# Kernel tuning notes

Measured on AMD Instinct MI355X. Metric: run time of the kernel, lower is better.

Reference implementation:

```python
import jax, jax.numpy as jnp
import numpy as np

N = 50000
E = 800000
D = 128
H = 8
DH = D // H


def setup_inputs() -> dict:
    key = jax.random.key(0)
    ks = jax.random.split(key, 8)
    x = jax.random.normal(ks[0], (N, D), dtype=jnp.float32)
    src = jax.random.randint(ks[1], (E,), 0, N, dtype=jnp.int32)
    dst = jax.random.randint(ks[2], (E,), 0, N, dtype=jnp.int32)
    s = 1.0 / np.sqrt(D)
    w_qkv = jax.random.uniform(ks[3], (3 * D, D), jnp.float32, -s, s)
    b_qkv = jax.random.uniform(ks[4], (3 * D,), jnp.float32, -s, s)
    w_out = jax.random.uniform(ks[5], (D, D), jnp.float32, -s, s)
    b_out = jax.random.uniform(ks[6], (D,), jnp.float32, -s, s)
    return {"x": x, "src": src, "dst": dst, "w_qkv": w_qkv, "b_qkv": b_qkv,
            "w_out": w_out, "b_out": b_out}


def reference(x, src, dst, w_qkv, b_qkv, w_out, b_out):
    n = x.shape[0]
    coef = 1.0 / np.sqrt(DH)
    qkv = (x @ w_qkv.T + b_qkv).reshape(n, H, 3 * DH)
    q, k, v = qkv[..., :DH], qkv[..., DH:2 * DH], qkv[..., 2 * DH:]
    # per-edge scores: dot(k[src], q[dst]) per head -> [E, H]
    scores = jnp.einsum('ehd,ehd->eh', k[src], q[dst]) * coef
    # edge softmax over edges sharing the same destination node
    smax = jax.ops.segment_max(scores, dst, num_segments=n)  # [N, H]
    smax = jnp.where(jnp.isfinite(smax), smax, 0.0)
    ex = jnp.exp(scores - smax[dst])                          # [E, H]
    denom = jax.ops.segment_sum(ex, dst, num_segments=n)      # [N, H]
    probs = ex / jnp.maximum(denom[dst], 1e-30)
    # weighted aggregation of source values -> [N, H, DH]
    agg = jax.ops.segment_sum(probs[:, :, None] * v[src], dst, num_segments=n)
    out = agg.reshape(n, D) @ w_out.T + b_out
    return out
```

## Files before the change

### kernel.cpp

```cpp
#include <hip/hip_runtime.h>
#include <math.h>

#define DD   128
#define NQKV 384
#define CAP  128

typedef __attribute__((ext_vector_type(8))) short          bf16x8;
typedef __attribute__((ext_vector_type(8))) unsigned short ushort8;
typedef __attribute__((ext_vector_type(4))) float          f32x4;

__device__ __forceinline__ unsigned short f2bf(float f) {
    unsigned u = __float_as_uint(f);
    u += 0x7fffu + ((u >> 16) & 1u);
    return (unsigned short)(u >> 16);
}
__device__ __forceinline__ float bf2f(unsigned short h) {
    return __uint_as_float(((unsigned)h) << 16);
}
__device__ __forceinline__ float bflo(unsigned u) { return __uint_as_float(u << 16); }
__device__ __forceinline__ float bfhi(unsigned u) { return __uint_as_float(u & 0xffff0000u); }

#define NWQ8 (NQKV * DD / 8)
#define NWO8 (DD * DD / 8)

__global__ void prep_kernel(const float* __restrict__ w_qkv, const float* __restrict__ w_out,
                            unsigned short* __restrict__ wq_hi, unsigned short* __restrict__ wq_lo,
                            unsigned short* __restrict__ wo_hi, unsigned short* __restrict__ wo_lo,
                            int* __restrict__ counts, int nzc4) {
    int i = blockIdx.x * blockDim.x + threadIdx.x;
    if (i < nzc4) {
        ((int4*)counts)[i] = make_int4(0, 0, 0, 0);
        return;
    }
    int j = i - nzc4;
    const float* srcp;
    unsigned short *hip_, *lop_;
    if (j < NWQ8)            { srcp = w_qkv + (size_t)j * 8;          hip_ = wq_hi + (size_t)j * 8;          lop_ = wq_lo + (size_t)j * 8; }
    else if (j < NWQ8+NWO8)  { int k = j - NWQ8; srcp = w_out + (size_t)k * 8; hip_ = wo_hi + (size_t)k * 8; lop_ = wo_lo + (size_t)k * 8; }
    else return;
    const float4* p = (const float4*)srcp;
    float4 a = p[0], b = p[1];
    float v[8] = {a.x, a.y, a.z, a.w, b.x, b.y, b.z, b.w};
    ushort8 vh, vl;
    #pragma unroll
    for (int t = 0; t < 8; ++t) {
        unsigned short h = f2bf(v[t]);
        vh[t] = h;
        vl[t] = f2bf(v[t] - bf2f(h));
    }
    *(ushort8*)hip_ = vh;
    *(ushort8*)lop_ = vl;
}

__global__ void scatter_fixed_kernel(const int* __restrict__ src, const int* __restrict__ dst,
                                     int* __restrict__ counts, int* __restrict__ lists, int E) {
    int t = blockIdx.x * blockDim.x + threadIdx.x;
    int base = t * 8;
    if (base >= E) return;
    if (base + 8 <= E) {
        int4 d0 = *(const int4*)(dst + base);
        int4 d1 = *(const int4*)(dst + base + 4);
        int4 s0 = *(const int4*)(src + base);
        int4 s1 = *(const int4*)(src + base + 4);
        int dd[8] = {d0.x, d0.y, d0.z, d0.w, d1.x, d1.y, d1.z, d1.w};
        int ss[8] = {s0.x, s0.y, s0.z, s0.w, s1.x, s1.y, s1.z, s1.w};
        int pos[8];
        #pragma unroll
        for (int i = 0; i < 8; ++i) pos[i] = atomicAdd(&counts[dd[i]], 1);
        #pragma unroll
        for (int i = 0; i < 8; ++i)
            if (pos[i] < CAP) lists[(size_t)dd[i] * CAP + pos[i]] = ss[i];
    } else {
        for (int e = base; e < E; ++e) {
            int d = dst[e];
            int pos = atomicAdd(&counts[d], 1);
            if (pos < CAP) lists[(size_t)d * CAP + pos] = src[e];
        }
    }
}

#define TM 128
#define TN 128
#define LDA 40

__global__ __launch_bounds__(256, 3) void qkv_gemm_kernel(
    const float* __restrict__ X,
    const unsigned short* __restrict__ Bh, const unsigned short* __restrict__ Bl,
    const float* __restrict__ bias, unsigned short* __restrict__ Cq,
    unsigned short* __restrict__ Ck, unsigned short* __restrict__ Cv, int M)
{
    __shared__ unsigned short As[TM * LDA];
    __shared__ unsigned short Bs_h[TN * LDA];
    __shared__ unsigned short Bs_l[TN * LDA];

    const int tid  = threadIdx.x;
    const int l    = tid & 63;
    const int wv   = tid >> 6;
    const int quad = l >> 4;
    const int l15  = l & 15;
    const int wm   = (wv & 1) * 64;
    const int wn   = (wv >> 1) * 64;
    const int n0   = blockIdx.x * TN;
    const int m0   = blockIdx.y * TM;

    f32x4 acc[4][4];
    #pragma unroll
    for (int i = 0; i < 4; ++i)
        #pragma unroll
        for (int j = 0; j < 4; ++j) acc[i][j] = (f32x4)0.f;

    #pragma unroll
    for (int kc = 0; kc < DD; kc += 32) {
        #pragma unroll
        for (int it = 0; it < 2; ++it) {
            int idx = tid + it * 256;
            int row = idx >> 2;
            int pc  = idx & 3;
            int loff = row * LDA + pc * 8;
            ushort8 va = 0;
            if (m0 + row < M) {
                const float4* xp = (const float4*)(X + (size_t)(m0 + row) * DD + kc + pc * 8);
                float4 a0 = xp[0], a1 = xp[1];
                float v[8] = {a0.x,a0.y,a0.z,a0.w,a1.x,a1.y,a1.z,a1.w};
                #pragma unroll
                for (int t = 0; t < 8; ++t) va[t] = f2bf(v[t]);
            }
            *(ushort8*)&As[loff] = va;
            size_t gb = (size_t)(n0 + row) * DD + kc + pc * 8;
            *(ushort8*)&Bs_h[loff] = *(const ushort8*)(Bh + gb);
            *(ushort8*)&Bs_l[loff] = *(const ushort8*)(Bl + gb);
        }
        __syncthreads();

        bf16x8 ah[4], bh[4], bl[4];
        #pragma unroll
        for (int mt = 0; mt < 4; ++mt)
            ah[mt] = *(const bf16x8*)&As[(wm + mt * 16 + l15) * LDA + quad * 8];
        #pragma unroll
        for (int nt = 0; nt < 4; ++nt) {
            int off = (wn + nt * 16 + l15) * LDA + quad * 8;
            bh[nt] = *(const bf16x8*)&Bs_h[off];
            bl[nt] = *(const bf16x8*)&Bs_l[off];
        }
        #pragma unroll
        for (int mt = 0; mt < 4; ++mt)
            #pragma unroll
            for (int nt = 0; nt < 4; ++nt) {
                acc[mt][nt] = __builtin_amdgcn_mfma_f32_16x16x32_bf16(ah[mt], bh[nt], acc[mt][nt], 0, 0, 0);
                acc[mt][nt] = __builtin_amdgcn_mfma_f32_16x16x32_bf16(ah[mt], bl[nt], acc[mt][nt], 0, 0, 0);
            }
        __syncthreads();
    }

    #pragma unroll
    for (int nt = 0; nt < 4; ++nt) {
        int j = n0 + wn + nt * 16 + l15;
        float bj = bias[j];
        int h = j / 48;
        int r = j - h * 48;
        int seg = (r >= 32) ? 2 : ((r >= 16) ? 1 : 0);
        int bc  = h * 16 + r - seg * 16;
        unsigned short* dstp = (seg == 0 ? Cq : (seg == 1 ? Ck : Cv));
        #pragma unroll
        for (int mt = 0; mt < 4; ++mt)
            #pragma unroll
            for (int rr = 0; rr < 4; ++rr) {
                int m = m0 + wm + mt * 16 + quad * 4 + rr;
                if (m < M) dstp[(size_t)m * DD + bc] = f2bf(acc[mt][nt][rr] + bj);
            }
    }
}

__global__ __launch_bounds__(256, 3) void out_gemm_kernel(
    const unsigned short* __restrict__ A,
    const unsigned short* __restrict__ Bh, const unsigned short* __restrict__ Bl,
    const float* __restrict__ bias, float* __restrict__ C, int M)
{
    __shared__ unsigned short As[TM * LDA];
    __shared__ unsigned short Bs_h[TN * LDA];
    __shared__ unsigned short Bs_l[TN * LDA];

    const int tid  = threadIdx.x;
    const int l    = tid & 63;
    const int wv   = tid >> 6;
    const int quad = l >> 4;
    const int l15  = l & 15;
    const int wm   = (wv & 1) * 64;
    const int wn   = (wv >> 1) * 64;
    const int m0   = blockIdx.x * TM;

    f32x4 acc[4][4];
    #pragma unroll
    for (int i = 0; i < 4; ++i)
        #pragma unroll
        for (int j = 0; j < 4; ++j) acc[i][j] = (f32x4)0.f;

    #pragma unroll
    for (int kc = 0; kc < DD; kc += 32) {
        #pragma unroll
        for (int it = 0; it < 2; ++it) {
            int idx = tid + it * 256;
            int row = idx >> 2;
            int pc  = idx & 3;
            int loff = row * LDA + pc * 8;
            ushort8 va = 0;
            if (m0 + row < M)
                va = *(const ushort8*)(A + (size_t)(m0 + row) * DD + kc + pc * 8);
            *(ushort8*)&As[loff] = va;
            size_t gb = (size_t)row * DD + kc + pc * 8;
            *(ushort8*)&Bs_h[loff] = *(const ushort8*)(Bh + gb);
            *(ushort8*)&Bs_l[loff] = *(const ushort8*)(Bl + gb);
        }
        __syncthreads();

        bf16x8 ah[4], bh[4], bl[4];
        #pragma unroll
        for (int mt = 0; mt < 4; ++mt)
            ah[mt] = *(const bf16x8*)&As[(wm + mt * 16 + l15) * LDA + quad * 8];
        #pragma unroll
        for (int nt = 0; nt < 4; ++nt) {
            int off = (wn + nt * 16 + l15) * LDA + quad * 8;
            bh[nt] = *(const bf16x8*)&Bs_h[off];
            bl[nt] = *(const bf16x8*)&Bs_l[off];
        }
        #pragma unroll
        for (int mt = 0; mt < 4; ++mt)
            #pragma unroll
            for (int nt = 0; nt < 4; ++nt) {
                acc[mt][nt] = __builtin_amdgcn_mfma_f32_16x16x32_bf16(ah[mt], bh[nt], acc[mt][nt], 0, 0, 0);
                acc[mt][nt] = __builtin_amdgcn_mfma_f32_16x16x32_bf16(ah[mt], bl[nt], acc[mt][nt], 0, 0, 0);
            }
        __syncthreads();
    }

    #pragma unroll
    for (int nt = 0; nt < 4; ++nt) {
        int j = wn + nt * 16 + l15;
        float bj = bias[j];
        #pragma unroll
        for (int mt = 0; mt < 4; ++mt)
            #pragma unroll
            for (int rr = 0; rr < 4; ++rr) {
                int m = m0 + wm + mt * 16 + quad * 4 + rr;
                if (m < M) C[(size_t)m * DD + j] = acc[mt][nt][rr] + bj;
            }
    }
}

__global__ __launch_bounds__(256) void wave_attn_kernel(
    const unsigned short* __restrict__ qbf, const unsigned short* __restrict__ kbf,
    const unsigned short* __restrict__ vbf, const int* __restrict__ lists,
    const int* __restrict__ counts,
    unsigned short* __restrict__ agg, int N)
{
    const int lane = threadIdx.x & 63;
    const int n = blockIdx.x * 4 + (threadIdx.x >> 6);
    if (n >= N) return;

    const int h = lane >> 3;
    const int e = lane & 7;

    const int deg = min(counts[n], CAP);
    const size_t obase = (size_t)n * DD + 2 * lane;
    if (deg == 0) {
        *(unsigned*)(agg + obase) = 0u;
        return;
    }

    const int row0 = n * CAP;

    const uint4* qp = (const uint4*)(qbf + (size_t)n * DD + h * 16);
    const uint4 qa = qp[0], qb = qp[1];
    const float4 q0 = make_float4(bflo(qa.x), bfhi(qa.x), bflo(qa.y), bfhi(qa.y));
    const float4 q1 = make_float4(bflo(qa.z), bfhi(qa.z), bflo(qa.w), bfhi(qa.w));
    const float4 q2 = make_float4(bflo(qb.x), bfhi(qb.x), bflo(qb.y), bfhi(qb.y));
    const float4 q3 = make_float4(bflo(qb.z), bfhi(qb.z), bflo(qb.w), bfhi(qb.w));

    int cur = lists[row0 + min(e, deg - 1)];
    int nxt = lists[row0 + min(8 + e, deg - 1)];

    const uint4* kp0 = (const uint4*)(kbf + (size_t)cur * DD + h * 16);
    uint4 ka = kp0[0], kb = kp0[1];
    unsigned vv[8];
    #pragma unroll
    for (int ee = 0; ee < 8; ++ee)
        vv[ee] = *(const unsigned*)(vbf + (size_t)__shfl(cur, ee) * DD + 2 * lane);

    float l_run = 0.f;
    float acc0 = 0.f, acc1 = 0.f;

    for (int c = 0; c < deg; c += 8) {
        const int cnt = min(8, deg - c);
        const bool more = (c + 8 < deg);

        const int nn = lists[row0 + min(c + 16 + e, deg - 1)];

        uint4 k1a = ka, k1b = kb;
        unsigned vn[8];
        #pragma unroll
        for (int ee = 0; ee < 8; ++ee) vn[ee] = vv[ee];
        if (more) {
            const uint4* kp = (const uint4*)(kbf + (size_t)nxt * DD + h * 16);
            k1a = kp[0]; k1b = kp[1];
            #pragma unroll
            for (int ee = 0; ee < 8; ++ee)
                vn[ee] = *(const unsigned*)(vbf + (size_t)__shfl(nxt, ee) * DD + 2 * lane);
        }

        float s = bflo(ka.x)*q0.x + bfhi(ka.x)*q0.y + bflo(ka.y)*q0.z + bfhi(ka.y)*q0.w
                + bflo(ka.z)*q1.x + bfhi(ka.z)*q1.y + bflo(ka.w)*q1.z + bfhi(ka.w)*q1.w
                + bflo(kb.x)*q2.x + bfhi(kb.x)*q2.y + bflo(kb.y)*q2.z + bfhi(kb.y)*q2.w
                + bflo(kb.z)*q3.x + bfhi(kb.z)*q3.y + bflo(kb.w)*q3.z + bfhi(kb.w)*q3.w;

        const float p = (e < cnt) ? __expf(s * 0.25f) : 0.f;
        l_run += p;

        #pragma unroll
        for (int ee = 0; ee < 8; ++ee) {
            const float pe = __shfl(p, (lane & 0x38) | ee);
            acc0 = fmaf(pe, bflo(vv[ee]), acc0);
            acc1 = fmaf(pe, bfhi(vv[ee]), acc1);
        }

        ka = k1a; kb = k1b;
        #pragma unroll
        for (int ee = 0; ee < 8; ++ee) vv[ee] = vn[ee];
        cur = nxt; nxt = nn;
    }

    l_run += __shfl_xor(l_run, 1);
    l_run += __shfl_xor(l_run, 2);
    l_run += __shfl_xor(l_run, 4);

    const float inv = 1.f / fmaxf(l_run, 1e-30f);
    const float o0 = acc0 * inv, o1 = acc1 * inv;
    *(unsigned*)(agg + obase) = (unsigned)f2bf(o0) | ((unsigned)f2bf(o1) << 16);
}

extern "C" void kernel_launch(void* const* d_in, const int* in_sizes, int n_in,
                              void* d_out, int out_size, void* d_ws, size_t ws_size,
                              hipStream_t stream) {
    const float* x     = (const float*)d_in[0];
    const int*   src   = (const int*)  d_in[1];
    const int*   dst   = (const int*)  d_in[2];
    const float* w_qkv = (const float*)d_in[3];
    const float* b_qkv = (const float*)d_in[4];
    const float* w_out = (const float*)d_in[5];
    const float* b_out = (const float*)d_in[6];
    float* out = (float*)d_out;

    const int N = in_sizes[0] / DD;
    const int E = in_sizes[1];

    typedef unsigned short u16;
    char* ws = (char*)d_ws;
    u16* qbf   = (u16*)ws;   ws += (size_t)N * DD * sizeof(u16);
    u16* kbf   = (u16*)ws;   ws += (size_t)N * DD * sizeof(u16);
    u16* vbf   = (u16*)ws;   ws += (size_t)N * DD * sizeof(u16);
    u16* aggb  = (u16*)ws;   ws += (size_t)N * DD * sizeof(u16);
    u16* wq_hi = (u16*)ws;   ws += (size_t)NQKV * DD * sizeof(u16);
    u16* wq_lo = (u16*)ws;   ws += (size_t)NQKV * DD * sizeof(u16);
    u16* wo_hi = (u16*)ws;   ws += (size_t)DD * DD * sizeof(u16);
    u16* wo_lo = (u16*)ws;   ws += (size_t)DD * DD * sizeof(u16);
    int* counts = (int*)ws;  ws += (size_t)((N + 3) / 4 * 4) * sizeof(int);
    int* lists  = (int*)ws;  ws += (size_t)N * CAP * sizeof(int);

    const int nzc4 = (N + 3) / 4;
    const int npb  = (nzc4 + NWQ8 + NWO8 + 255) / 256;
    const int nsb  = ((E + 7) / 8 + 255) / 256;
    const int MB   = (N + TM - 1) / TM;

    prep_kernel<<<npb, 256, 0, stream>>>(w_qkv, w_out, wq_hi, wq_lo, wo_hi, wo_lo,
                                         counts, nzc4);
    scatter_fixed_kernel<<<nsb, 256, 0, stream>>>(src, dst, counts, lists, E);

    qkv_gemm_kernel<<<dim3(NQKV / TN, MB), 256, 0, stream>>>(
        x, wq_hi, wq_lo, b_qkv, qbf, kbf, vbf, N);

    wave_attn_kernel<<<(N + 3) / 4, 256, 0, stream>>>(
        qbf, kbf, vbf, lists, counts, aggb, N);

    out_gemm_kernel<<<MB, 256, 0, stream>>>(
        aggb, wo_hi, wo_lo, b_out, out, N);
}
```

Before: 240.5 us.

## Make edge attention kernel persistent with ping-pong buffers and split accumulators

The attention kernel becomes a grid-stride persistent kernel with a fixed 2048 blocks, each wave looping over several destination nodes instead of one node per wave. The main loop is manually unrolled into two steps that alternate between two K/V register buffers, which removes the per-iteration register copies. The score dot product is split into four independent FMA chains, and the value accumulators are split into even and odd pairs to shorten dependency chains. Addressing moves to 32-bit byte offsets. The risks are higher register pressure from the duplicated buffers and load imbalance from the fixed grid size.

```diff
diff --git a/kernel.cpp b/kernel.cpp
--- a/kernel.cpp
+++ b/kernel.cpp
@@ -247,94 +247,132 @@
     }
 }
 
+#define ATTN_BLOCKS 2048
+
+#define ATTN_STEP(cka, ckb, cvv, nka, nkb, nvv)                                   \
+  {                                                                                \
+    const int cnt  = min(8, deg - c);                                              \
+    const bool more = (c + 8 < deg);                                               \
+    const int nn = lists[row0 + min(c + 16 + e, deg - 1)];                         \
+    if (more) {                                                                    \
+      const unsigned koff = (((unsigned)nxt) << 8) + hoff;                         \
+      nka = *(const uint4*)(kb8 + koff);                                           \
+      nkb = *(const uint4*)(kb8 + koff + 16);                                      \
+      _Pragma("unroll")                                                            \
+      for (int ee = 0; ee < 8; ++ee)                                               \
+        nvv[ee] = *(const unsigned*)(vb8 + ((((unsigned)__shfl(nxt, ee)) << 8) + loff4)); \
+    }                                                                              \
+                                           \
+    float sA = bflo(cka.x) * q0.x;                                                 \
+    sA = fmaf(bfhi(cka.x), q0.y, sA);                                              \
+    sA = fmaf(bflo(cka.y), q0.z, sA);                                              \
+    sA = fmaf(bfhi(cka.y), q0.w, sA);                                              \
+    float sB = bflo(cka.z) * q1.x;                                                 \
+    sB = fmaf(bfhi(cka.z), q1.y, sB);                                              \
+    sB = fmaf(bflo(cka.w), q1.z, sB);                                              \
+    sB = fmaf(bfhi(cka.w), q1.w, sB);                                              \
+    float sC = bflo(ckb.x) * q2.x;                                                 \
+    sC = fmaf(bfhi(ckb.x), q2.y, sC);                                              \
+    sC = fmaf(bflo(ckb.y), q2.z, sC);                                              \
+    sC = fmaf(bfhi(ckb.y), q2.w, sC);                                              \
+    float sD = bflo(ckb.z) * q3.x;                                                 \
+    sD = fmaf(bfhi(ckb.z), q3.y, sD);                                              \
+    sD = fmaf(bflo(ckb.w), q3.z, sD);                                              \
+    sD = fmaf(bfhi(ckb.w), q3.w, sD);                                              \
+    const float s_ = (sA + sB) + (sC + sD);                                        \
+    const float pp = __expf(s_ * 0.25f);                           \
+    const float p_ = (e < cnt) ? pp : 0.f;                                         \
+    l_run += p_;                                                                   \
+    _Pragma("unroll")                                                              \
+    for (int ee = 0; ee < 8; ++ee) {                                               \
+      const float pe = __shfl(p_, lbase | ee);          \
+      if ((ee & 1) == 0) {                                                         \
+        acc0a = fmaf(pe, bflo(cvv[ee]), acc0a);                                    \
+        acc1a = fmaf(pe, bfhi(cvv[ee]), acc1a);                                    \
+      } else {                                                                     \
+        acc0b = fmaf(pe, bflo(cvv[ee]), acc0b);                                    \
+        acc1b = fmaf(pe, bfhi(cvv[ee]), acc1b);                                    \
+      }                                                                            \
+    }                                                                              \
+    nxt = nn;                                                                      \
+    c += 8;                                                                        \
+  }
+
 __global__ __launch_bounds__(256) void wave_attn_kernel(
     const unsigned short* __restrict__ qbf, const unsigned short* __restrict__ kbf,
     const unsigned short* __restrict__ vbf, const int* __restrict__ lists,
     const int* __restrict__ counts,
     unsigned short* __restrict__ agg, int N)
 {
-    const int lane = threadIdx.x & 63;
-    const int n = blockIdx.x * 4 + (threadIdx.x >> 6);
-    if (n >= N) return;
+    const int lane   = threadIdx.x & 63;
+    const int wid    = blockIdx.x * 4 + (threadIdx.x >> 6);
+    const int nwaves = gridDim.x * 4;
 
     const int h = lane >> 3;
     const int e = lane & 7;
-
-    const int deg = min(counts[n], CAP);
-    const size_t obase = (size_t)n * DD + 2 * lane;
-    if (deg == 0) {
-        *(unsigned*)(agg + obase) = 0u;
-        return;
-    }
-
-    const int row0 = n * CAP;
-
-    const uint4* qp = (const uint4*)(qbf + (size_t)n * DD + h * 16);
-    const uint4 qa = qp[0], qb = qp[1];
-    const float4 q0 = make_float4(bflo(qa.x), bfhi(qa.x), bflo(qa.y), bfhi(qa.y));
-    const float4 q1 = make_float4(bflo(qa.z), bfhi(qa.z), bflo(qa.w), bfhi(qa.w));
-    const float4 q2 = make_float4(bflo(qb.x), bfhi(qb.x), bflo(qb.y), bfhi(qb.y));
-    const float4 q3 = make_float4(bflo(qb.z), bfhi(qb.z), bflo(qb.w), bfhi(qb.w));
-
-    int cur = lists[row0 + min(e, deg - 1)];
-    int nxt = lists[row0 + min(8 + e, deg - 1)];
-
-    const uint4* kp0 = (const uint4*)(kbf + (size_t)cur * DD + h * 16);
-    uint4 ka = kp0[0], kb = kp0[1];
-    unsigned vv[8];
-    #pragma unroll
-    for (int ee = 0; ee < 8; ++ee)
-        vv[ee] = *(const unsigned*)(vbf + (size_t)__shfl(cur, ee) * DD + 2 * lane);
-
-    float l_run = 0.f;
-    float acc0 = 0.f, acc1 = 0.f;
-
-    for (int c = 0; c < deg; c += 8) {
-        const int cnt = min(8, deg - c);
-        const bool more = (c + 8 < deg);
-
-        const int nn = lists[row0 + min(c + 16 + e, deg - 1)];
-
-        uint4 k1a = ka, k1b = kb;
-        unsigned vn[8];
-        #pragma unroll
-        for (int ee = 0; ee < 8; ++ee) vn[ee] = vv[ee];
-        if (more) {
-            const uint4* kp = (const uint4*)(kbf + (size_t)nxt * DD + h * 16);
-            k1a = kp[0]; k1b = kp[1];
+    const unsigned hoff  = (unsigned)h << 5;
+    const unsigned loff4 = (unsigned)lane << 2;
+    const int lbase = lane & 0x38;
+
+    const char* kb8 = (const char*)kbf;
+    const char* vb8 = (const char*)vbf;
+    const char* qb8 = (const char*)qbf;
+    char*       ab8 = (char*)agg;
+
+    for (int n = wid; n < N; n += nwaves) {
+        const int deg = min(counts[n], CAP);
+        const unsigned ooff = (((unsigned)n) << 8) + loff4;
+        if (deg == 0) {
+            *(unsigned*)(ab8 + ooff) = 0u;
+            continue;
+        }
+
+        const int row0 = n * CAP;
+
+        const unsigned qoff = (((unsigned)n) << 8) + hoff;
+        const uint4 qa = *(const uint4*)(qb8 + qoff);
+        const uint4 qb = *(const uint4*)(qb8 + qoff + 16);
+        const float4 q0 = make_float4(bflo(qa.x), bfhi(qa.x), bflo(qa.y), bfhi(qa.y));
+        const float4 q1 = make_float4(bflo(qa.z), bfhi(qa.z), bflo(qa.w), bfhi(qa.w));
+        const float4 q2 = make_float4(bflo(qb.x), bfhi(qb.x), bflo(qb.y), bfhi(qb.y));
+        const float4 q3 = make_float4(bflo(qb.z), bfhi(qb.z), bflo(qb.w), bfhi(qb.w));
+
+        const int c0s = lists[row0 + min(e, deg - 1)];
+        int nxt = lists[row0 + min(8 + e, deg - 1)];
+
+        uint4 ka0, kb0, ka1, kb1;
+        unsigned vv0[8], vv1[8];
+        {
+            const unsigned koff = (((unsigned)c0s) << 8) + hoff;
+            ka0 = *(const uint4*)(kb8 + koff);
+            kb0 = *(const uint4*)(kb8 + koff + 16);
             #pragma unroll
             for (int ee = 0; ee < 8; ++ee)
-                vn[ee] = *(const unsigned*)(vbf + (size_t)__shfl(nxt, ee) * DD + 2 * lane);
-        }
-
-        float s = bflo(ka.x)*q0.x + bfhi(ka.x)*q0.y + bflo(ka.y)*q0.z + bfhi(ka.y)*q0.w
-                + bflo(ka.z)*q1.x + bfhi(ka.z)*q1.y + bflo(ka.w)*q1.z + bfhi(ka.w)*q1.w
-                + bflo(kb.x)*q2.x + bfhi(kb.x)*q2.y + bflo(kb.y)*q2.z + bfhi(kb.y)*q2.w
-                + bflo(kb.z)*q3.x + bfhi(kb.z)*q3.y + bflo(kb.w)*q3.z + bfhi(kb.w)*q3.w;
-
-        const float p = (e < cnt) ? __expf(s * 0.25f) : 0.f;
-        l_run += p;
-
-        #pragma unroll
-        for (int ee = 0; ee < 8; ++ee) {
-            const float pe = __shfl(p, (lane & 0x38) | ee);
-            acc0 = fmaf(pe, bflo(vv[ee]), acc0);
-            acc1 = fmaf(pe, bfhi(vv[ee]), acc1);
-        }
-
-        ka = k1a; kb = k1b;
-        #pragma unroll
-        for (int ee = 0; ee < 8; ++ee) vv[ee] = vn[ee];
-        cur = nxt; nxt = nn;
-    }
-
-    l_run += __shfl_xor(l_run, 1);
-    l_run += __shfl_xor(l_run, 2);
-    l_run += __shfl_xor(l_run, 4);
-
-    const float inv = 1.f / fmaxf(l_run, 1e-30f);
-    const float o0 = acc0 * inv, o1 = acc1 * inv;
-    *(unsigned*)(agg + obase) = (unsigned)f2bf(o0) | ((unsigned)f2bf(o1) << 16);
+                vv0[ee] = *(const unsigned*)(vb8 + ((((unsigned)__shfl(c0s, ee)) << 8) + loff4));
+        }
+        ka1 = ka0; kb1 = kb0;
+        #pragma unroll
+        for (int ee = 0; ee < 8; ++ee) vv1[ee] = 0u;
+
+        float l_run = 0.f;
+        float acc0a = 0.f, acc0b = 0.f, acc1a = 0.f, acc1b = 0.f;
+
+        int c = 0;
+        for (;;) {
+            ATTN_STEP(ka0, kb0, vv0, ka1, kb1, vv1);
+            if (c >= deg) break;
+            ATTN_STEP(ka1, kb1, vv1, ka0, kb0, vv0);
+            if (c >= deg) break;
+        }
+
+        l_run += __shfl_xor(l_run, 1);
+        l_run += __shfl_xor(l_run, 2);
+        l_run += __shfl_xor(l_run, 4);
+
+        const float inv = 1.f / fmaxf(l_run, 1e-30f);
+        const float o0 = (acc0a + acc0b) * inv, o1 = (acc1a + acc1b) * inv;
+        *(unsigned*)(ab8 + ooff) = (unsigned)f2bf(o0) | ((unsigned)f2bf(o1) << 16);
+    }
 }
 
 extern "C" void kernel_launch(void* const* d_in, const int* in_sizes, int n_in,
@@ -377,7 +415,7 @@
     qkv_gemm_kernel<<<dim3(NQKV / TN, MB), 256, 0, stream>>>(
         x, wq_hi, wq_lo, b_qkv, qbf, kbf, vbf, N);
 
-    wave_attn_kernel<<<(N + 3) / 4, 256, 0, stream>>>(
+    wave_attn_kernel<<<ATTN_BLOCKS, 256, 0, stream>>>(
         qbf, kbf, vbf, lists, counts, aggb, N);
 
     out_gemm_kernel<<<MB, 256, 0, stream>>>(
```

Result: no change. 240.3 us (-0.1%).
